# Performance work log

Measured on AMD Instinct MI355X. Metric: run time of the kernel, lower is better.

## Reference

```python
import jax, jax.numpy as jnp
import numpy as np

ALPHA, GAMMA = 0.25, 2.0            # focal loss params (cfg defaults)
W_CLASS, W_BBOX, W_GIOU = 2.0, 5.0, 2.0
N_CANDIDATE_K = 5                   # top-k ious used to derive dynamic k
CENTER_RADIUS = 2.5
B, Q, G, C = 32, 2000, 64, 80
IMG_W, IMG_H = 1333.0, 800.0


def _box_iou(a, b):
    # a: [Q,4] xyxy, b: [G,4] xyxy -> iou [Q,G], union [Q,G]
    area_a = (a[:, 2] - a[:, 0]) * (a[:, 3] - a[:, 1])
    area_b = (b[:, 2] - b[:, 0]) * (b[:, 3] - b[:, 1])
    lt = jnp.maximum(a[:, None, :2], b[None, :, :2])
    rb = jnp.minimum(a[:, None, 2:], b[None, :, 2:])
    wh = jnp.clip(rb - lt, 0.0)
    inter = wh[..., 0] * wh[..., 1]
    union = area_a[:, None] + area_b[None, :] - inter
    return inter / union, union


def _generalized_box_iou(a, b):
    iou, union = _box_iou(a, b)
    lt = jnp.minimum(a[:, None, :2], b[None, :, :2])
    rb = jnp.maximum(a[:, None, 2:], b[None, :, 2:])
    wh = jnp.clip(rb - lt, 0.0)
    area_c = wh[..., 0] * wh[..., 1]
    return iou - (area_c - union) / area_c


def _get_in_boxes_info(boxes, gt):
    # boxes, gt: absolute xyxy. Anchor centers inside gt box / inside center region.
    cx = (boxes[:, 0] + boxes[:, 2]) * 0.5
    cy = (boxes[:, 1] + boxes[:, 3]) * 0.5
    is_in_boxes = ((cx[:, None] > gt[None, :, 0]) & (cx[:, None] < gt[None, :, 2]) &
                   (cy[:, None] > gt[None, :, 1]) & (cy[:, None] < gt[None, :, 3]))
    gt_cx = (gt[:, 0] + gt[:, 2]) * 0.5
    gt_cy = (gt[:, 1] + gt[:, 3]) * 0.5
    gt_w = gt[:, 2] - gt[:, 0]
    gt_h = gt[:, 3] - gt[:, 1]
    is_in_centers = ((cx[:, None] > (gt_cx - CENTER_RADIUS * gt_w)[None, :]) &
                     (cx[:, None] < (gt_cx + CENTER_RADIUS * gt_w)[None, :]) &
                     (cy[:, None] > (gt_cy - CENTER_RADIUS * gt_h)[None, :]) &
                     (cy[:, None] < (gt_cy + CENTER_RADIUS * gt_h)[None, :]))
    fg_mask = is_in_boxes.any(1) | is_in_centers.any(1)
    return fg_mask, is_in_boxes & is_in_centers


def _dedup(cost, matching):
    # queries matched to >1 gt keep only their min-cost gt
    over = matching.sum(1) > 1
    keep = jax.nn.one_hot(jnp.argmin(cost, axis=1), cost.shape[1], dtype=matching.dtype)
    return jnp.where(over[:, None], keep, matching)


def _dynamic_k_matching(cost, ious):
    Qn, Gn = cost.shape
    topk_ious = jax.lax.top_k(ious.T, N_CANDIDATE_K)[0]              # [G,k]
    dynamic_ks = jnp.maximum(topk_ious.sum(1).astype(jnp.int32), 1)  # [G]
    # rank of each query within each gt's cost column (ascending)
    ranks = jnp.argsort(jnp.argsort(cost, axis=0), axis=0)
    matching = (ranks < dynamic_ks[None, :]).astype(cost.dtype)      # [Q,G]
    matching = _dedup(cost, matching)

    # ensure every gt gets >=1 query; bounded loop replaces data-dependent while
    def body(_, carry):
        cost_c, match_c = carry
        unmatched = match_c.sum(0) == 0                              # [G]
        any_un = unmatched.any()
        matched_q = match_c.sum(1) > 0
        cost_n = cost_c + jnp.where(matched_q, 1e5, 0.0)[:, None]
        add = jax.nn.one_hot(jnp.argmin(cost_n, axis=0), Qn, dtype=match_c.dtype).T
        match_n = jnp.maximum(match_c, add * unmatched[None, :].astype(match_c.dtype))
        match_n = _dedup(cost_n, match_n)
        return (jnp.where(any_un, cost_n, cost_c), jnp.where(any_un, match_n, match_c))

    cost, matching = jax.lax.fori_loop(0, Gn, body, (cost, matching))
    masked = jnp.where(matching > 0, cost, jnp.inf)
    matched_query_id = jnp.argmin(masked, axis=0)                    # [G]
    return matching, matched_query_id


def _match_one(logits, boxes, tgt_ids, gt_boxes, size_out, size_tgt):
    fg_mask, in_bc = _get_in_boxes_info(boxes, gt_boxes)
    ious, _ = _box_iou(boxes, gt_boxes)                              # [Q,G]
    neg = (1.0 - ALPHA) * logits ** GAMMA * (-jnp.log(1.0 - logits + 1e-8))
    pos = ALPHA * (1.0 - logits) ** GAMMA * (-jnp.log(logits + 1e-8))
    cost_class = jnp.take(pos - neg, tgt_ids, axis=1)                # [Q,G]
    out_n = boxes / size_out                                         # [Q,4]
    tgt_n = gt_boxes / size_tgt                                      # [G,4]
    cost_bbox = jnp.abs(out_n[:, None, :] - tgt_n[None, :, :]).sum(-1)  # L1 cdist
    cost_giou = -_generalized_box_iou(boxes, gt_boxes)
    cost = (W_BBOX * cost_bbox + W_CLASS * cost_class + W_GIOU * cost_giou
            + 100.0 * (~in_bc).astype(cost_bbox.dtype))
    cost = cost + jnp.where(fg_mask, 0.0, 1e4)[:, None]
    return _dynamic_k_matching(cost, ious)


def _rand_boxes(key, n_shape):
    k1, k2 = jax.random.split(key)
    wh = jnp.array([IMG_W, IMG_H], jnp.float32)
    ctr = jax.random.uniform(k1, n_shape + (2,)) * wh
    size = jax.random.uniform(k2, n_shape + (2,)) * (wh * 0.3) + 8.0
    x1y1 = jnp.clip(ctr - size * 0.5, 0.0, wh)
    x2y2 = jnp.clip(ctr + size * 0.5, 0.0, wh)
    x2y2 = jnp.maximum(x2y2, x1y1 + 1.0)
    return jnp.concatenate([x1y1, x2y2], axis=-1)


def setup_inputs() -> dict:
    key = jax.random.key(0)
    k1, k2, k3, k4 = jax.random.split(key, 4)
    pred_logits = jax.random.uniform(k1, (B, Q, C), minval=1e-4, maxval=1.0 - 1e-4)
    pred_boxes = _rand_boxes(k2, (B, Q))
    gt_classes = jax.random.randint(k3, (B, G), 0, C)
    gt_boxes = _rand_boxes(k4, (B, G))
    sz = jnp.array([IMG_W, IMG_H, IMG_W, IMG_H], jnp.float32)
    return {
        'pred_logits': pred_logits,
        'pred_boxes': pred_boxes,
        'gt_classes': gt_classes,
        'gt_boxes': gt_boxes,
        'image_size_xyxy': jnp.tile(sz, (B, 1)),
        'image_size_xyxy_tgt': jnp.tile(sz, (B, G, 1)),
    }


def reference(pred_logits, pred_boxes, gt_classes, gt_boxes, image_size_xyxy, image_size_xyxy_tgt):
    # matching: [B,Q,G] 0/1 assignment matrix (row q matched to gt g);
    # matched_query_id: [B,G] best query per gt. Padded-G, fixed-shape analog of
    # the per-image variable-length (indices, matched_ids) lists.
    matching, matched_query_id = jax.vmap(_match_one)(
        pred_logits, pred_boxes, gt_classes, gt_boxes, image_size_xyxy, image_size_xyxy_tgt)
    return matching, matched_query_id
```

## Files before the change

kernel.cpp:

```cpp
#include <hip/hip_runtime.h>
#include <cmath>

#pragma clang fp contract(off)

#define BB 32
#define QQ 2000
#define GG 64
#define CCH 80
#define TOPC 16

typedef unsigned long long u64;

__global__ __launch_bounds__(256) void cost_kernel(
    const float* __restrict__ logits, const float* __restrict__ boxes,
    const int* __restrict__ gtc, const float* __restrict__ gtb,
    const float* __restrict__ szout, const float* __restrict__ sztgt,
    float* __restrict__ cost, int* __restrict__ rowarg,
    float* __restrict__ out_match) {
#pragma clang fp contract(off)
  const int b = blockIdx.y;
  const int q0 = blockIdx.x * 64;
  const int t = threadIdx.x;
  const int w = t >> 6, lane = t & 63;

  __shared__ float4 s_qb[64];
  __shared__ float s_tile[64 * 65];

  const int gbase = (b * GG + lane) * 4;
  const float g0 = gtb[gbase + 0], g1 = gtb[gbase + 1];
  const float g2 = gtb[gbase + 2], g3 = gtb[gbase + 3];
  const float t0 = g0 / sztgt[gbase + 0], t1 = g1 / sztgt[gbase + 1];
  const float t2 = g2 / sztgt[gbase + 2], t3 = g3 / sztgt[gbase + 3];
  const float garea = (g2 - g0) * (g3 - g1);
  const float gcx = (g0 + g2) * 0.5f, gcy = (g1 + g3) * 0.5f;
  const float gw = g2 - g0, gh = g3 - g1;
  const float cxlo = gcx - 2.5f * gw, cxhi = gcx + 2.5f * gw;
  const float cylo = gcy - 2.5f * gh, cyhi = gcy + 2.5f * gh;
  const int cls = gtc[b * GG + lane];
  const float so0 = szout[b * 4 + 0], so1 = szout[b * 4 + 1];
  const float so2 = szout[b * 4 + 2], so3 = szout[b * 4 + 3];

  if (t < 64) {
    int q = q0 + t;
    s_qb[t] = (q < QQ) ? reinterpret_cast<const float4*>(boxes)[b * QQ + q]
                       : make_float4(0.f, 0.f, 1.f, 1.f);
  }
  __syncthreads();

  const float* lbase = logits + (size_t)b * QQ * CCH;
  for (int i = 0; i < 16; ++i) {
    const int qi = w * 16 + i;
    const int q = q0 + qi;
    float4 bx = s_qb[qi];
    float x1 = bx.x, y1 = bx.y, x2 = bx.z, y2 = bx.w;
    float on0 = x1 / so0, on1 = y1 / so1, on2 = x2 / so2, on3 = y2 / so3;
    float cx = (x1 + x2) * 0.5f, cy = (y1 + y2) * 0.5f;
    float areaa = (x2 - x1) * (y2 - y1);

    bool ib = (cx > g0) & (cx < g2) & (cy > g1) & (cy < g3);
    bool ic = (cx > cxlo) & (cx < cxhi) & (cy > cylo) & (cy < cyhi);
    bool fg = (__ballot(ib) != 0ull) || (__ballot(ic) != 0ull);
    float fgadd = fg ? 0.0f : 1e4f;

    float ltx = fmaxf(x1, g0), lty = fmaxf(y1, g1);
    float rbx = fminf(x2, g2), rby = fminf(y2, g3);
    float iw = fmaxf(rbx - ltx, 0.0f), ih = fmaxf(rby - lty, 0.0f);
    float inter = iw * ih;
    float uni = (areaa + garea) - inter;
    float iou = inter / uni;
    float ex1 = fminf(x1, g0), ey1 = fminf(y1, g1);
    float ex2 = fmaxf(x2, g2), ey2 = fmaxf(y2, g3);
    float ew = fmaxf(ex2 - ex1, 0.0f), eh = fmaxf(ey2 - ey1, 0.0f);
    float areac = ew * eh;
    float giou = iou - (areac - uni) / areac;

    float p = (q < QQ) ? lbase[(size_t)q * CCH + cls] : 0.5f;
    float negc = (0.75f * (p * p)) * (-logf((1.0f - p) + 1e-8f));
    float posc = (0.25f * ((1.0f - p) * (1.0f - p))) * (-logf(p + 1e-8f));
    float ccls = posc - negc;

    float cb = ((fabsf(on0 - t0) + fabsf(on1 - t1)) + fabsf(on2 - t2)) + fabsf(on3 - t3);
    float notbc = (ib & ic) ? 0.0f : 1.0f;
    float c = ((5.0f * cb + 2.0f * ccls) + 2.0f * (-giou)) + 100.0f * notbc;
    c = c + fgadd;

    s_tile[qi * 65 + lane] = c;

    float bv = c; int bg = lane;
    for (int off = 32; off; off >>= 1) {
      float ov = __shfl_down(bv, off, 64); int og = __shfl_down(bg, off, 64);
      if (ov < bv || (ov == bv && og < bg)) { bv = ov; bg = og; }
    }
    if (lane == 0 && q < QQ) rowarg[b * QQ + q] = bg;
  }
  __syncthreads();

  float* cb_out = cost + (size_t)b * GG * QQ;
  const int qi = t & 63;
  const int q = q0 + qi;
  if (q < QQ) {
    #pragma unroll
    for (int pass = 0; pass < 16; ++pass) {
      int g = (t >> 6) + pass * 4;
      cb_out[(size_t)g * QQ + q] = s_tile[qi * 65 + g];
    }
  }

  int nq = QQ - q0; if (nq > 64) nq = 64;
  if (nq > 0) {
    float4* zb = reinterpret_cast<float4*>(out_match + ((size_t)b * QQ + q0) * GG);
    int n4 = nq * GG / 4;
    float4 z = make_float4(0.f, 0.f, 0.f, 0.f);
    for (int i = t; i < n4; i += 256) zb[i] = z;
  }
}

template <int TOPN>
__device__ __forceinline__ void block_select(
    u64 (&K)[8], int tid, u64* s_tmin, u64* s_cmin, u64* s_surv,
    u64* s_sorted, u64* s_thr, int* s_ns) {
  u64 m = K[0];
  #pragma unroll
  for (int j = 1; j < 8; ++j) m = (K[j] < m) ? K[j] : m;
  s_tmin[tid] = m;
  if (tid == 0) *s_ns = 0;
  __syncthreads();

  if (tid < 64) {
    u64 c = s_tmin[tid];
    u64 c1 = s_tmin[tid + 64], c2 = s_tmin[tid + 128], c3 = s_tmin[tid + 192];
    c = (c1 < c) ? c1 : c; c = (c2 < c) ? c2 : c; c = (c3 < c) ? c3 : c;
    s_cmin[tid] = c;
    int r = 0;
    for (int j = 0; j < 64; ++j) r += (s_cmin[j] < c) ? 1 : 0;
    if (r == TOPN - 1) *s_thr = c;
  }
  __syncthreads();

  const u64 t = *s_thr;
  int n = 0;
  #pragma unroll
  for (int j = 0; j < 8; ++j) n += (K[j] <= t) ? 1 : 0;
  if (n) {
    int base = atomicAdd(s_ns, n);
    int k = 0;
    #pragma unroll
    for (int j = 0; j < 8; ++j) if (K[j] <= t) s_surv[base + (k++)] = K[j];
  }
  __syncthreads();

  const int ns = *s_ns;
  if (ns <= 64) {
    if (tid < ns && tid < 64) {
      u64 k = s_surv[tid];
      int r = 0;
      for (int j = 0; j < ns; ++j) r += (s_surv[j] < k) ? 1 : 0;
      if (r < TOPN) s_sorted[r] = k;
    }
  } else if (tid < 64) {
    for (int pass = 0; pass < TOPN; ++pass) {
      u64 bk = ~0ull;
      for (int idx = tid; idx < ns; idx += 64) {
        u64 v = s_surv[idx]; bk = (v < bk) ? v : bk;
      }
      for (int off = 32; off; off >>= 1) {
        u64 ok = __shfl_down(bk, off, 64); bk = (ok < bk) ? ok : bk;
      }
      bk = __shfl(bk, 0, 64);
      for (int idx = tid; idx < ns; idx += 64)
        if (s_surv[idx] == bk) s_surv[idx] = ~0ull;
      if (tid == 0) s_sorted[pass] = bk;
    }
  }
  __syncthreads();
}

__global__ __launch_bounds__(256) void pick_kernel(
    const float* __restrict__ boxes, const float* __restrict__ gtb,
    const float* __restrict__ cost, short* __restrict__ lists,
    int* __restrict__ dynks) {
#pragma clang fp contract(off)
  const int bc = blockIdx.x;
  const int b = bc >> 6, col = bc & 63;
  const int tid = threadIdx.x;

  __shared__ u64 s_tmin[256];
  __shared__ u64 s_cmin[64];
  __shared__ u64 s_surv[512];
  __shared__ u64 s_sorted[TOPC];
  __shared__ u64 s_thr;
  __shared__ int s_ns;

  const int gbase = (b * GG + col) * 4;
  const float gx1 = gtb[gbase + 0], gy1 = gtb[gbase + 1];
  const float gx2 = gtb[gbase + 2], gy2 = gtb[gbase + 3];
  const float ga = (gx2 - gx1) * (gy2 - gy1);

  u64 K[8];
  #pragma unroll
  for (int j = 0; j < 8; ++j) {
    int q = tid * 8 + j;
    float val = -1e30f;
    if (q < QQ) {
      float4 bx = reinterpret_cast<const float4*>(boxes)[b * QQ + q];
      float areaa = (bx.z - bx.x) * (bx.w - bx.y);
      float ltx = fmaxf(bx.x, gx1), lty = fmaxf(bx.y, gy1);
      float rbx = fminf(bx.z, gx2), rby = fminf(bx.w, gy2);
      float iw = fmaxf(rbx - ltx, 0.0f), ih = fmaxf(rby - lty, 0.0f);
      float inter = iw * ih;
      val = inter / ((areaa + ga) - inter);
    }
    unsigned u = __float_as_uint(val);
    u = (u & 0x80000000u) ? ~u : (u | 0x80000000u);
    K[j] = ~(((u64)u << 16) | (u64)(0xFFFF - q));
  }
  block_select<5>(K, tid, s_tmin, s_cmin, s_surv, s_sorted, &s_thr, &s_ns);
  if (tid == 0) {
    float s = 0.0f;
    for (int r = 0; r < 5; ++r) {
      u64 kk = ~s_sorted[r];
      unsigned u = (unsigned)(kk >> 16);
      u = (u & 0x80000000u) ? (u & 0x7FFFFFFFu) : ~u;
      s += __uint_as_float(u);
    }
    int dynk = (int)s;
    if (dynk < 1) dynk = 1;
    dynks[bc] = dynk;
  }

  const float* ccol = cost + (size_t)bc * QQ;
  {
    float cv[8];
    if (tid < 249) {
      const float4* c4 = reinterpret_cast<const float4*>(ccol) + tid * 2;
      float4 a = c4[0], d = c4[1];
      cv[0] = a.x; cv[1] = a.y; cv[2] = a.z; cv[3] = a.w;
      cv[4] = d.x; cv[5] = d.y; cv[6] = d.z; cv[7] = d.w;
    } else {
      #pragma unroll
      for (int j = 0; j < 8; ++j) {
        int q = tid * 8 + j;
        cv[j] = (q < QQ) ? ccol[q] : INFINITY;
      }
    }
    #pragma unroll
    for (int j = 0; j < 8; ++j) {
      unsigned u = __float_as_uint(cv[j]);
      u = (u & 0x80000000u) ? ~u : (u | 0x80000000u);
      K[j] = ((u64)u << 16) | (u64)(tid * 8 + j);
    }
  }
  block_select<TOPC>(K, tid, s_tmin, s_cmin, s_surv, s_sorted, &s_thr, &s_ns);
  if (tid < TOPC) lists[bc * TOPC + tid] = (short)(s_sorted[tid] & 0xFFFFull);
}

__global__ __launch_bounds__(256) void serial_kernel(
    const float* __restrict__ cost, const short* __restrict__ lists,
    const int* __restrict__ dynks, const int* __restrict__ rowarg,
    float* __restrict__ out_match, float* __restrict__ out_ids) {
#pragma clang fp contract(off)
  const int b = blockIdx.x;
  const int tid = threadIdx.x;

  __shared__ unsigned s_mlo[QQ], s_mhi[QQ];
  __shared__ int s_first[QQ];
  __shared__ int s_pushed[QQ];
  __shared__ short s_rarg[QQ];
  __shared__ short s_list[GG * TOPC];
  __shared__ int s_cnt[GG];
  __shared__ short s_chosen[GG];
  __shared__ unsigned long long s_pack[GG];
  __shared__ int s_added[GG];
  __shared__ short s_ucols[GG];
  __shared__ short s_fb[GG];
  __shared__ int s_nadd, s_nfb, s_Tv;

  for (int q = tid; q < QQ; q += 256) {
    s_mlo[q] = 0u; s_mhi[q] = 0u; s_first[q] = -1; s_pushed[q] = -1;
    s_rarg[q] = (short)rowarg[b * QQ + q];
  }
  for (int i = tid; i < GG * TOPC; i += 256) s_list[i] = lists[b * GG * TOPC + i];
  if (tid < GG) s_cnt[tid] = 0;
  __syncthreads();

  if (tid < GG) {
    int dynk = dynks[b * GG + tid];
    s_cnt[tid] = dynk;
    for (int i = 0; i < dynk; ++i) {
      int q = s_list[tid * TOPC + i];
      if (tid < 32) atomicOr(&s_mlo[q], 1u << tid);
      else          atomicOr(&s_mhi[q], 1u << (tid - 32));
      s_first[q] = 0;
    }
  }
  __syncthreads();

  for (int q = tid; q < QQ; q += 256) {
    unsigned lo = s_mlo[q], hi = s_mhi[q];
    if (__popc(lo) + __popc(hi) > 1) {
      int bg = s_rarg[q];
      unsigned tl = lo, th = hi;
      while (tl) { int g = __ffs(tl) - 1; tl &= tl - 1; if (g != bg) atomicSub(&s_cnt[g], 1); }
      while (th) { int g = __ffs(th) + 31; th &= th - 1; if (g != bg) atomicSub(&s_cnt[g], 1); }
      bool had = (bg < 32) ? ((lo >> bg) & 1u) : ((hi >> (bg - 32)) & 1u);
      if (!had) atomicAdd(&s_cnt[bg], 1);
      s_mlo[q] = (bg < 32) ? (1u << bg) : 0u;
      s_mhi[q] = (bg >= 32) ? (1u << (bg - 32)) : 0u;
    }
  }
  __syncthreads();

  const float* costb = cost + (size_t)b * GG * QQ;

  if (tid < 64) {
    const int lane = tid;
    int T = 0;
    for (int iter = 0; iter < GG; ++iter) {
      unsigned long long bal = __ballot(s_cnt[lane] > 0);
      unsigned long long um = ~bal;
      if (um == 0ull) break;
      T++;

      bool isun = (um >> lane) & 1ull;
      int nu = __popcll(um);
      int pos = __popcll(um & ((1ull << lane) - 1ull));
      if (isun) s_ucols[pos] = (short)lane;
      if (lane == 0) { s_nfb = 0; s_nadd = 0; }

      const int sg = lane >> 4, li = lane & 15;
      for (int base = 0; base < nu; base += 4) {
        int ci = base + sg;
        int col = (ci < nu) ? (int)s_ucols[ci] : -1;
        bool cand_un = false; int cq = 0;
        if (col >= 0) {
          cq = s_list[col * TOPC + li];
          cand_un = ((s_mlo[cq] | s_mhi[cq]) == 0u);
        }
        unsigned long long bb = __ballot(cand_un);
        unsigned sub = (unsigned)((bb >> (sg * 16)) & 0xFFFFull);
        if (col >= 0) {
          if (sub) {
            if (li == __ffs(sub) - 1) s_chosen[col] = (short)cq;
          } else if (li == 0) {
            int slot = atomicAdd(&s_nfb, 1);
            s_fb[slot] = (short)col;
          }
        }
      }

      int nfb = s_nfb;
      for (int fi = 0; fi < nfb; ++fi) {
        int col = s_fb[fi];
        const float* ccol = costb + (size_t)col * QQ;
        float bv = INFINITY; int bq = 0x7fffffff;
        for (int q2 = lane; q2 < QQ; q2 += 64) {
          if ((s_mlo[q2] | s_mhi[q2]) == 0u) {
            float cv = ccol[q2];
            if (cv < bv) { bv = cv; bq = q2; }
          }
        }
        for (int off = 32; off; off >>= 1) {
          float ov = __shfl_down(bv, off, 64); int oq = __shfl_down(bq, off, 64);
          if (ov < bv || (ov == bv && oq < bq)) { bv = ov; bq = oq; }
        }
        bq = __shfl(bq, 0, 64);
        if (bq == 0x7fffffff) {
          bv = INFINITY; bq = 0x7fffffff;
          for (int q2 = lane; q2 < QQ; q2 += 64) {
            float cv = ccol[q2];
            int k = (s_first[q2] >= 0) ? (iter + 1 - s_first[q2]) : 0;
            for (int tt = 0; tt < k; ++tt) cv += 1e5f;
            if (cv < bv) { bv = cv; bq = q2; }
          }
          for (int off = 32; off; off >>= 1) {
            float ov = __shfl_down(bv, off, 64); int oq = __shfl_down(bq, off, 64);
            if (ov < bv || (ov == bv && oq < bq)) { bv = ov; bq = oq; }
          }
          bq = __shfl(bq, 0, 64);
        }
        if (lane == 0) s_chosen[col] = (short)bq;
      }

      if (isun) {
        int q = s_chosen[lane];
        if (lane < 32) atomicOr(&s_mlo[q], 1u << lane);
        else           atomicOr(&s_mhi[q], 1u << (lane - 32));
        atomicAdd(&s_cnt[lane], 1);
        if (s_first[q] == -1) s_first[q] = iter + 1;
        if (atomicExch(&s_pushed[q], iter) != iter) {
          int slot = atomicAdd(&s_nadd, 1);
          s_added[slot] = q;
        }
      }

      int na = s_nadd;
      if (lane < na) {
        int q = s_added[lane];
        unsigned lo = s_mlo[q], hi = s_mhi[q];
        if (__popc(lo) + __popc(hi) > 1) {
          int bg = s_rarg[q];
          unsigned tl = lo, th = hi;
          while (tl) { int g = __ffs(tl) - 1; tl &= tl - 1; if (g != bg) atomicSub(&s_cnt[g], 1); }
          while (th) { int g = __ffs(th) + 31; th &= th - 1; if (g != bg) atomicSub(&s_cnt[g], 1); }
          bool had = (bg < 32) ? ((lo >> bg) & 1u) : ((hi >> (bg - 32)) & 1u);
          if (!had) atomicAdd(&s_cnt[bg], 1);
          s_mlo[q] = (bg < 32) ? (1u << bg) : 0u;
          s_mhi[q] = (bg >= 32) ? (1u << (bg - 32)) : 0u;
        }
      }
    }
    if (tid == 0) s_Tv = T;
  }
  __syncthreads();
  const int T = s_Tv;

  if (tid < GG) s_pack[tid] = 0xFFFFFFFFFFFFFFFFull;
  __syncthreads();
  for (int q = tid; q < QQ; q += 256) {
    unsigned lo = s_mlo[q], hi = s_mhi[q];
    if (lo | hi) {
      int g = lo ? (__ffs(lo) - 1) : (__ffs(hi) + 31);
      float cv = costb[(size_t)g * QQ + q];
      int k = T - s_first[q];
      for (int tt = 0; tt < k; ++tt) cv += 1e5f;
      unsigned ub = __float_as_uint(cv);
      ub = (ub & 0x80000000u) ? ~ub : (ub | 0x80000000u);
      unsigned long long pk = ((unsigned long long)ub << 16) | (unsigned)q;
      atomicMin(&s_pack[g], pk);
    }
  }
  __syncthreads();
  if (tid < GG) {
    unsigned long long pk = s_pack[tid];
    out_ids[b * GG + tid] =
        (pk == 0xFFFFFFFFFFFFFFFFull) ? 0.0f : (float)(pk & 0xFFFFull);
  }
  for (int q = tid; q < QQ; q += 256) {
    unsigned lo = s_mlo[q], hi = s_mhi[q];
    if (lo | hi) {
      int g = lo ? (__ffs(lo) - 1) : (__ffs(hi) + 31);
      out_match[((size_t)b * QQ + q) * GG + g] = 1.0f;
    }
  }
}

extern "C" void kernel_launch(void* const* d_in, const int* in_sizes, int n_in,
                              void* d_out, int out_size, void* d_ws, size_t ws_size,
                              hipStream_t stream) {
  const float* logits = (const float*)d_in[0];
  const float* boxes  = (const float*)d_in[1];
  const int*   gtc    = (const int*)d_in[2];
  const float* gtbx   = (const float*)d_in[3];
  const float* szout  = (const float*)d_in[4];
  const float* sztgt  = (const float*)d_in[5];
  float* out = (float*)d_out;

  const size_t matchN  = (size_t)BB * QQ * GG;
  const size_t rowargN = (size_t)BB * QQ;
  const size_t listsN  = (size_t)BB * GG * TOPC;

  char* p = (char*)d_ws;
  float* cost   = (float*)p;          p += matchN * 4;
  int*   rowarg = (int*)p;            p += rowargN * 4;
  short* lists  = (short*)p;          p += listsN * 2;
  int*   dynks  = (int*)p;

  float* out_ids = out + matchN;

  hipLaunchKernelGGL(cost_kernel, dim3(32, BB), dim3(256), 0, stream,
                     logits, boxes, gtc, gtbx, szout, sztgt, cost, rowarg, out);
  hipLaunchKernelGGL(pick_kernel, dim3(BB * GG), dim3(256), 0, stream,
                     boxes, gtbx, cost, lists, dynks);
  hipLaunchKernelGGL(serial_kernel, dim3(BB), dim3(256), 0, stream,
                     cost, lists, dynks, rowarg, out, out_ids);
}
```

Before: 138.7 us.

## Halve cost_kernel query tile, prefetch logits, precompute normalized boxes, serial row argmin

Shrinks the query tile per block from 64 to 32, doubling the grid of cost_kernel for better occupancy. The logits gathers are hoisted into a register array issued before the barrier so their latency overlaps, and normalized query boxes are computed once per query in shared memory. The per-query wavefront shuffle argmin is replaced by a serial scan over the shared tile by 32 threads after the barrier. This trades shuffle work for a serialized loop done by only half a wave, and more blocks mean more redundant loading of GT parameters.

```diff
diff --git a/kernel.cpp b/kernel.cpp
--- a/kernel.cpp
+++ b/kernel.cpp
@@ -8,6 +8,7 @@
 #define GG 64
 #define CCH 80
 #define TOPC 16
+#define QT 32
 
 typedef unsigned long long u64;
 
@@ -19,12 +20,13 @@
     float* __restrict__ out_match) {
 #pragma clang fp contract(off)
   const int b = blockIdx.y;
-  const int q0 = blockIdx.x * 64;
+  const int q0 = blockIdx.x * QT;
   const int t = threadIdx.x;
   const int w = t >> 6, lane = t & 63;
 
-  __shared__ float4 s_qb[64];
-  __shared__ float s_tile[64 * 65];
+  __shared__ float4 s_qb[QT];
+  __shared__ float4 s_qn[QT];
+  __shared__ float s_tile[QT * 65];
 
   const int gbase = (b * GG + lane) * 4;
   const float g0 = gtb[gbase + 0], g1 = gtb[gbase + 1];
@@ -37,23 +39,35 @@
   const float cxlo = gcx - 2.5f * gw, cxhi = gcx + 2.5f * gw;
   const float cylo = gcy - 2.5f * gh, cyhi = gcy + 2.5f * gh;
   const int cls = gtc[b * GG + lane];
-  const float so0 = szout[b * 4 + 0], so1 = szout[b * 4 + 1];
-  const float so2 = szout[b * 4 + 2], so3 = szout[b * 4 + 3];
-
-  if (t < 64) {
+
+  if (t < QT) {
     int q = q0 + t;
-    s_qb[t] = (q < QQ) ? reinterpret_cast<const float4*>(boxes)[b * QQ + q]
-                       : make_float4(0.f, 0.f, 1.f, 1.f);
-  }
-  __syncthreads();
+    float4 bx = (q < QQ) ? reinterpret_cast<const float4*>(boxes)[b * QQ + q]
+                         : make_float4(0.f, 0.f, 1.f, 1.f);
+    s_qb[t] = bx;
+    float4 on;
+    on.x = bx.x / szout[b * 4 + 0];
+    on.y = bx.y / szout[b * 4 + 1];
+    on.z = bx.z / szout[b * 4 + 2];
+    on.w = bx.w / szout[b * 4 + 3];
+    s_qn[t] = on;
+  }
 
   const float* lbase = logits + (size_t)b * QQ * CCH;
-  for (int i = 0; i < 16; ++i) {
-    const int qi = w * 16 + i;
-    const int q = q0 + qi;
+  float pv[8];
+  #pragma unroll
+  for (int i = 0; i < 8; ++i) {
+    int q = q0 + w * 8 + i;
+    pv[i] = (q < QQ) ? lbase[(size_t)q * CCH + cls] : 0.5f;
+  }
+  __syncthreads();
+
+  #pragma unroll
+  for (int i = 0; i < 8; ++i) {
+    const int qi = w * 8 + i;
     float4 bx = s_qb[qi];
+    float4 on = s_qn[qi];
     float x1 = bx.x, y1 = bx.y, x2 = bx.z, y2 = bx.w;
-    float on0 = x1 / so0, on1 = y1 / so1, on2 = x2 / so2, on3 = y2 / so3;
     float cx = (x1 + x2) * 0.5f, cy = (y1 + y2) * 0.5f;
     float areaa = (x2 - x1) * (y2 - y1);
 
@@ -74,39 +88,46 @@
     float areac = ew * eh;
     float giou = iou - (areac - uni) / areac;
 
-    float p = (q < QQ) ? lbase[(size_t)q * CCH + cls] : 0.5f;
+    float p = pv[i];
     float negc = (0.75f * (p * p)) * (-logf((1.0f - p) + 1e-8f));
     float posc = (0.25f * ((1.0f - p) * (1.0f - p))) * (-logf(p + 1e-8f));
     float ccls = posc - negc;
 
-    float cb = ((fabsf(on0 - t0) + fabsf(on1 - t1)) + fabsf(on2 - t2)) + fabsf(on3 - t3);
+    float cb = ((fabsf(on.x - t0) + fabsf(on.y - t1)) + fabsf(on.z - t2)) + fabsf(on.w - t3);
     float notbc = (ib & ic) ? 0.0f : 1.0f;
     float c = ((5.0f * cb + 2.0f * ccls) + 2.0f * (-giou)) + 100.0f * notbc;
     c = c + fgadd;
 
     s_tile[qi * 65 + lane] = c;
-
-    float bv = c; int bg = lane;
-    for (int off = 32; off; off >>= 1) {
-      float ov = __shfl_down(bv, off, 64); int og = __shfl_down(bg, off, 64);
-      if (ov < bv || (ov == bv && og < bg)) { bv = ov; bg = og; }
-    }
-    if (lane == 0 && q < QQ) rowarg[b * QQ + q] = bg;
-  }
-  __syncthreads();
+  }
+  __syncthreads();
+
+  if (t < QT) {
+    int q = q0 + t;
+    if (q < QQ) {
+      const float* row = &s_tile[t * 65];
+      float bv = row[0]; int bg = 0;
+      #pragma unroll
+      for (int g = 1; g < GG; ++g) {
+        float cv = row[g];
+        if (cv < bv) { bv = cv; bg = g; }
+      }
+      rowarg[b * QQ + q] = bg;
+    }
+  }
 
   float* cb_out = cost + (size_t)b * GG * QQ;
-  const int qi = t & 63;
+  const int qi = t & 31;
   const int q = q0 + qi;
   if (q < QQ) {
     #pragma unroll
-    for (int pass = 0; pass < 16; ++pass) {
-      int g = (t >> 6) + pass * 4;
+    for (int pass = 0; pass < 8; ++pass) {
+      int g = (t >> 5) + pass * 8;
       cb_out[(size_t)g * QQ + q] = s_tile[qi * 65 + g];
     }
   }
 
-  int nq = QQ - q0; if (nq > 64) nq = 64;
+  int nq = QQ - q0; if (nq > QT) nq = QT;
   if (nq > 0) {
     float4* zb = reinterpret_cast<float4*>(out_match + ((size_t)b * QQ + q0) * GG);
     int n4 = nq * GG / 4;
@@ -467,7 +488,7 @@
 
   float* out_ids = out + matchN;
 
-  hipLaunchKernelGGL(cost_kernel, dim3(32, BB), dim3(256), 0, stream,
+  hipLaunchKernelGGL(cost_kernel, dim3((QQ + QT - 1) / QT, BB), dim3(256), 0, stream,
                      logits, boxes, gtc, gtbx, szout, sztgt, cost, rowarg, out);
   hipLaunchKernelGGL(pick_kernel, dim3(BB * GG), dim3(256), 0, stream,
                      boxes, gtbx, cost, lists, dynks);
```

Measured after the change: 127.6 us. 1.09x faster.
